# Performance work log

Measured on AMD Instinct MI355X. Metric: run time of the kernel, lower is better.

The kernel has to match this reference:

```python
import jax, jax.numpy as jnp
import numpy as np

N_NODES = 100000
N_EDGES = 640000
IN_FEATS = 128
OUT_FEATS = 128


def setup_inputs() -> dict:
    key = jax.random.key(0)
    k1, k2, k3, k4 = jax.random.split(key, 4)
    feature = jax.random.normal(k1, (N_NODES, IN_FEATS), dtype=jnp.float32)
    edge_index = jax.random.randint(k2, (2, N_EDGES), 0, N_NODES, dtype=jnp.int64)
    # Linear params (W stored as [in, out] so out = h @ W + b, same math as torch Linear)
    W = jax.random.normal(k3, (IN_FEATS, OUT_FEATS), dtype=jnp.float32) / np.sqrt(IN_FEATS)
    b = jax.random.normal(k4, (OUT_FEATS,), dtype=jnp.float32) * 0.01
    return {"feature": feature, "edge_index": edge_index, "W": W, "b": b}


def reference(feature, edge_index, W, b):
    src, dst = edge_index[0], edge_index[1]
    # copy_src: gather source-node features along edges -> [E, in]
    msgs = feature[src]
    # sum reduce at destination nodes -> [N, in]
    h = jax.ops.segment_sum(msgs, dst, num_segments=N_NODES)
    # post-aggregation linear
    return h @ W + b
```

## Files before the change

### kernel.cpp

```cpp
#include <hip/hip_runtime.h>

#define N_NODES 100000
#define N_EDGES 640000
#define FEATS   128
#define CAP     32
#define LDSK    136

typedef __attribute__((ext_vector_type(8))) short short8;
typedef __attribute__((ext_vector_type(4))) float f32x4;

static __device__ __forceinline__ unsigned short f2bf(float f) {
  union { float f; unsigned u; } c; c.f = f;
  unsigned u = c.u + 0x7fffu + ((c.u >> 16) & 1u);
  return (unsigned short)(u >> 16);
}
static __device__ __forceinline__ float asf(unsigned u) {
  union { unsigned u; float f; } c; c.u = u;
  return c.f;
}

__global__ __launch_bounds__(256) void init_prep(
    const float* __restrict__ W, int* __restrict__ cnt,
    unsigned short* __restrict__ WT) {
  int b = blockIdx.x;
  if (b < 782) {
    int i = b * 256 + threadIdx.x;
    if (i < 2 * N_NODES) cnt[i] = 0;
  } else {
    int g = (b - 782) * 256 + threadIdx.x;
    int k = g >> 7, n = g & 127;
    WT[n * 128 + k] = f2bf(W[g]);
  }
}

__global__ __launch_bounds__(256) void bucket_edges(
    const int* __restrict__ edge,
    int* __restrict__ cntA, int* __restrict__ bucket) {
  int t     = blockIdx.x;
  int cls   = t & 7;
  int q     = t >> 3;
  int shard = q & 1;
  int base  = (q >> 1) * 2048 + shard * 1024;
  int* cnt  = cntA + shard * N_NODES;
  int* bkt  = bucket + (size_t)shard * 32 * N_NODES;
  #pragma unroll
  for (int k = 0; k < 4; ++k) {
    int e = base + k * 256 + threadIdx.x;
    if (e < N_EDGES) {
      int d = edge[N_EDGES + e];
      if (((d >> 4) & 7) == cls) {
        int s = edge[e];
        int slot = atomicAdd(&cnt[d], 1);
        if (slot < CAP) bkt[(size_t)slot * N_NODES + d] = s;
      }
    }
  }
}

__global__ __launch_bounds__(256) void gemm_g(
    const float* __restrict__ feature, const unsigned short* __restrict__ WT,
    unsigned short* __restrict__ g_bf) {
  __shared__ unsigned short WTs[128 * LDSK];

  #pragma unroll
  for (int i = 0; i < 8; ++i) {
    int c = threadIdx.x + i * 256;
    int n = c >> 4, j = c & 15;
    *(short8*)&WTs[n * LDSK + j * 8] = *(const short8*)(WT + n * 128 + j * 8);
  }
  __syncthreads();

  const int w    = threadIdx.x >> 6;
  const int lane = threadIdx.x & 63;
  const int ln15 = lane & 15;
  const int quad = lane >> 4;
  const int node_base = blockIdx.x * 128 + w * 32;

  f32x4 acc[2][8] = {};

  #pragma unroll
  for (int kb = 0; kb < 4; ++kb) {
    int kofs = kb * 32 + quad * 8;
    int n0 = min(node_base + ln15,      N_NODES - 1);
    int n1 = min(node_base + 16 + ln15, N_NODES - 1);
    const float* p0 = feature + (size_t)n0 * FEATS + kofs;
    const float* p1 = feature + (size_t)n1 * FEATS + kofs;
    float4 x0 = *(const float4*)p0, x1 = *(const float4*)(p0 + 4);
    float4 y0 = *(const float4*)p1, y1 = *(const float4*)(p1 + 4);
    unsigned short ua[8] = {f2bf(x0.x), f2bf(x0.y), f2bf(x0.z), f2bf(x0.w),
                            f2bf(x1.x), f2bf(x1.y), f2bf(x1.z), f2bf(x1.w)};
    unsigned short ub[8] = {f2bf(y0.x), f2bf(y0.y), f2bf(y0.z), f2bf(y0.w),
                            f2bf(y1.x), f2bf(y1.y), f2bf(y1.z), f2bf(y1.w)};
    short8 b0 = *(const short8*)ua;
    short8 b1 = *(const short8*)ub;
    #pragma unroll
    for (int ct = 0; ct < 8; ++ct) {
      short8 aa = *(const short8*)&WTs[(ct * 16 + ln15) * LDSK + kofs];
      acc[0][ct] = __builtin_amdgcn_mfma_f32_16x16x32_bf16(aa, b0, acc[0][ct], 0, 0, 0);
      acc[1][ct] = __builtin_amdgcn_mfma_f32_16x16x32_bf16(aa, b1, acc[1][ct], 0, 0, 0);
    }
  }

  #pragma unroll
  for (int nt = 0; nt < 2; ++nt) {
    int node = node_base + nt * 16 + ln15;
    if (node < N_NODES) {
      #pragma unroll
      for (int j = 0; j < 4; ++j) {
        unsigned short q[8] = {
            f2bf(acc[nt][2 * j][0]),     f2bf(acc[nt][2 * j][1]),
            f2bf(acc[nt][2 * j][2]),     f2bf(acc[nt][2 * j][3]),
            f2bf(acc[nt][2 * j + 1][0]), f2bf(acc[nt][2 * j + 1][1]),
            f2bf(acc[nt][2 * j + 1][2]), f2bf(acc[nt][2 * j + 1][3])};
        *(uint4*)(g_bf + (size_t)node * FEATS + (j * 4 + quad) * 8) =
            *(const uint4*)q;
      }
    }
  }
}

#define ROW(i) ((i) < cA ? (i) : (i) - cA + 32)

__global__ __launch_bounds__(256) void gather_out(
    const unsigned short* __restrict__ g,
    const int* __restrict__ cntA, const int* __restrict__ bucket,
    const float* __restrict__ bias,
    float* __restrict__ out) {
  int gi   = blockIdx.x * 256 + threadIdx.x;
  int node = gi >> 4;
  int lane = gi & 15;
  int cA   = min(cntA[node], CAP);
  int cB   = min(cntA[N_NODES + node], CAP);
  int deg  = cA + cB;
  const int* eb = bucket + node;

  float a0 = 0.f, a1 = 0.f, a2 = 0.f, a3 = 0.f;
  float a4 = 0.f, a5 = 0.f, a6 = 0.f, a7 = 0.f;

  int i = 0;
  for (; i + 3 < deg; i += 4) {
    int s0 = eb[(size_t)ROW(i + 0) * N_NODES];
    int s1 = eb[(size_t)ROW(i + 1) * N_NODES];
    int s2 = eb[(size_t)ROW(i + 2) * N_NODES];
    int s3 = eb[(size_t)ROW(i + 3) * N_NODES];
    uint4 p0 = *(const uint4*)(g + (size_t)s0 * FEATS + lane * 8);
    uint4 p1 = *(const uint4*)(g + (size_t)s1 * FEATS + lane * 8);
    uint4 p2 = *(const uint4*)(g + (size_t)s2 * FEATS + lane * 8);
    uint4 p3 = *(const uint4*)(g + (size_t)s3 * FEATS + lane * 8);
    a0 += asf(p0.x << 16) + asf(p1.x << 16) + asf(p2.x << 16) + asf(p3.x << 16);
    a1 += asf(p0.x & 0xffff0000u) + asf(p1.x & 0xffff0000u) + asf(p2.x & 0xffff0000u) + asf(p3.x & 0xffff0000u);
    a2 += asf(p0.y << 16) + asf(p1.y << 16) + asf(p2.y << 16) + asf(p3.y << 16);
    a3 += asf(p0.y & 0xffff0000u) + asf(p1.y & 0xffff0000u) + asf(p2.y & 0xffff0000u) + asf(p3.y & 0xffff0000u);
    a4 += asf(p0.z << 16) + asf(p1.z << 16) + asf(p2.z << 16) + asf(p3.z << 16);
    a5 += asf(p0.z & 0xffff0000u) + asf(p1.z & 0xffff0000u) + asf(p2.z & 0xffff0000u) + asf(p3.z & 0xffff0000u);
    a6 += asf(p0.w << 16) + asf(p1.w << 16) + asf(p2.w << 16) + asf(p3.w << 16);
    a7 += asf(p0.w & 0xffff0000u) + asf(p1.w & 0xffff0000u) + asf(p2.w & 0xffff0000u) + asf(p3.w & 0xffff0000u);
  }
  for (; i < deg; ++i) {
    int s = eb[(size_t)ROW(i) * N_NODES];
    uint4 p = *(const uint4*)(g + (size_t)s * FEATS + lane * 8);
    a0 += asf(p.x << 16);
    a1 += asf(p.x & 0xffff0000u);
    a2 += asf(p.y << 16);
    a3 += asf(p.y & 0xffff0000u);
    a4 += asf(p.z << 16);
    a5 += asf(p.z & 0xffff0000u);
    a6 += asf(p.w << 16);
    a7 += asf(p.w & 0xffff0000u);
  }

  int c4 = (lane >> 2) * 8 + (lane & 3);
  float4 b0 = *((const float4*)bias + c4);
  float4 b1 = *((const float4*)bias + c4 + 4);
  f32x4 o0 = {a0 + b0.x, a1 + b0.y, a2 + b0.z, a3 + b0.w};
  f32x4 o1 = {a4 + b1.x, a5 + b1.y, a6 + b1.z, a7 + b1.w};
  f32x4* base = (f32x4*)(out + (size_t)node * FEATS);
  __builtin_nontemporal_store(o0, base + c4);
  __builtin_nontemporal_store(o1, base + c4 + 4);
}


extern "C" void kernel_launch(void* const* d_in, const int* in_sizes, int n_in,
                              void* d_out, int out_size, void* d_ws, size_t ws_size,
                              hipStream_t stream) {
  const float* feature = (const float*)d_in[0];
  const int*   edge    = (const int*)d_in[1];
  const float* W       = (const float*)d_in[2];
  const float* bias    = (const float*)d_in[3];
  float*       out     = (float*)d_out;

  char* ws = (char*)d_ws;
  int* cnt    = (int*)(ws);
  int* bucket = (int*)(ws + (1 << 20));
  unsigned short* WT   = (unsigned short*)(ws + (27 << 20));
  unsigned short* g_bf = (unsigned short*)(ws + (28 << 20));

  init_prep<<<846, 256, 0, stream>>>(W, cnt, WT);

  bucket_edges<<<313 * 8 * 2, 256, 0, stream>>>(edge, cnt, bucket);

  gemm_g<<<(N_NODES + 127) / 128, 256, 0, stream>>>(feature, WT, g_bf);

  gather_out<<<N_NODES * 16 / 256, 256, 0, stream>>>(
      g_bf, cnt, bucket, bias, out);
}
```

Baseline: 172.5 us.

## Fuse edge bucketing and feature GEMM into one interleaved launch with swizzled LDS

Merges the edge-bucketing kernel and the bf16 MFMA GEMM kernel into a single launch. Blocks are interleaved, 16 bucketing blocks and 8 GEMM slots per group, so the atomic-bound scatter and the compute-bound GEMM can run concurrently on the GPU. This removes one launch boundary and the serialization between the two independent stages. The padded LDS layout for W^T is replaced with an XOR swizzle, which shrinks shared memory while avoiding bank conflicts. In exchange, every block reserves the 32KB LDS even when it only buckets edges, which may limit occupancy for those blocks.

```diff
diff --git a/kernel.cpp b/kernel.cpp
--- a/kernel.cpp
+++ b/kernel.cpp
@@ -4,10 +4,11 @@
 #define N_EDGES 640000
 #define FEATS   128
 #define CAP     32
-#define LDSK    136
 
 typedef __attribute__((ext_vector_type(8))) short short8;
 typedef __attribute__((ext_vector_type(4))) float f32x4;
+
+#define SWZ(row, kofs) (((row) << 7) + ((((kofs) >> 3) ^ ((row) & 7)) << 3))
 
 static __device__ __forceinline__ unsigned short f2bf(float f) {
   union { float f; unsigned u; } c; c.f = f;
@@ -33,40 +34,46 @@
   }
 }
 
-__global__ __launch_bounds__(256) void bucket_edges(
+__global__ __launch_bounds__(256) void bucket_gemm(
+    const float* __restrict__ feature, const unsigned short* __restrict__ WT,
     const int* __restrict__ edge,
-    int* __restrict__ cntA, int* __restrict__ bucket) {
-  int t     = blockIdx.x;
-  int cls   = t & 7;
-  int q     = t >> 3;
-  int shard = q & 1;
-  int base  = (q >> 1) * 2048 + shard * 1024;
-  int* cnt  = cntA + shard * N_NODES;
-  int* bkt  = bucket + (size_t)shard * 32 * N_NODES;
-  #pragma unroll
-  for (int k = 0; k < 4; ++k) {
-    int e = base + k * 256 + threadIdx.x;
-    if (e < N_EDGES) {
-      int d = edge[N_EDGES + e];
-      if (((d >> 4) & 7) == cls) {
-        int s = edge[e];
-        int slot = atomicAdd(&cnt[d], 1);
-        if (slot < CAP) bkt[(size_t)slot * N_NODES + d] = s;
+    int* __restrict__ cntA, int* __restrict__ bucket,
+    unsigned short* __restrict__ g_bf) {
+  __shared__ unsigned short WTs[128 * 128];
+
+  int b  = blockIdx.x;
+  int sg = b / 24;
+  int r  = b - sg * 24;
+
+  if (r < 16) {
+    int cls   = r & 7;
+    int shard = r >> 3;
+    int base  = sg * 2048 + shard * 1024;
+    int* cnt  = cntA + shard * N_NODES;
+    int* bkt  = bucket + (size_t)shard * 32 * N_NODES;
+    #pragma unroll
+    for (int k = 0; k < 4; ++k) {
+      int e = base + k * 256 + threadIdx.x;
+      if (e < N_EDGES) {
+        int d = edge[N_EDGES + e];
+        if (((d >> 4) & 7) == cls) {
+          int s = edge[e];
+          int slot = atomicAdd(&cnt[d], 1);
+          if (slot < CAP) bkt[(size_t)slot * N_NODES + d] = s;
+        }
       }
     }
-  }
-}
-
-__global__ __launch_bounds__(256) void gemm_g(
-    const float* __restrict__ feature, const unsigned short* __restrict__ WT,
-    unsigned short* __restrict__ g_bf) {
-  __shared__ unsigned short WTs[128 * LDSK];
+    return;
+  }
+
+  int idx = (r - 16) * 313 + sg;
+  if (idx >= 782) return;
 
   #pragma unroll
   for (int i = 0; i < 8; ++i) {
     int c = threadIdx.x + i * 256;
     int n = c >> 4, j = c & 15;
-    *(short8*)&WTs[n * LDSK + j * 8] = *(const short8*)(WT + n * 128 + j * 8);
+    *(short8*)&WTs[SWZ(n, j * 8)] = *(const short8*)(WT + n * 128 + j * 8);
   }
   __syncthreads();
 
@@ -74,7 +81,7 @@
   const int lane = threadIdx.x & 63;
   const int ln15 = lane & 15;
   const int quad = lane >> 4;
-  const int node_base = blockIdx.x * 128 + w * 32;
+  const int node_base = idx * 128 + w * 32;
 
   f32x4 acc[2][8] = {};
 
@@ -95,7 +102,7 @@
     short8 b1 = *(const short8*)ub;
     #pragma unroll
     for (int ct = 0; ct < 8; ++ct) {
-      short8 aa = *(const short8*)&WTs[(ct * 16 + ln15) * LDSK + kofs];
+      short8 aa = *(const short8*)&WTs[SWZ(ct * 16 + ln15, kofs)];
       acc[0][ct] = __builtin_amdgcn_mfma_f32_16x16x32_bf16(aa, b0, acc[0][ct], 0, 0, 0);
       acc[1][ct] = __builtin_amdgcn_mfma_f32_16x16x32_bf16(aa, b1, acc[1][ct], 0, 0, 0);
     }
@@ -197,9 +204,8 @@
 
   init_prep<<<846, 256, 0, stream>>>(W, cnt, WT);
 
-  bucket_edges<<<313 * 8 * 2, 256, 0, stream>>>(edge, cnt, bucket);
-
-  gemm_g<<<(N_NODES + 127) / 128, 256, 0, stream>>>(feature, WT, g_bf);
+  bucket_gemm<<<313 * 24, 256, 0, stream>>>(
+      feature, WT, edge, cnt, bucket, g_bf);
 
   gather_out<<<N_NODES * 16 / 256, 256, 0, stream>>>(
       g_bf, cnt, bucket, bias, out);
```

After: 203.9 us. 18.2% more time.
